# Optimization experiments

Hardware: AMD Instinct MI355X
Metric: run time of the kernel (lower is better)

Reference implementation:

```python
import jax, jax.numpy as jnp
import numpy as np

EMBED_DIM = 1024
NUM_HEADS = 16
HEAD_DIM = EMBED_DIM // NUM_HEADS


def setup_inputs() -> dict:
    key = jax.random.key(0)
    ks = jax.random.split(key, 9)
    B, T, C = 4, 2048, EMBED_DIM
    s = 1.0 / np.sqrt(C)
    return {
        "x": jax.random.normal(ks[0], (B, T, C), jnp.float32),
        "Wq": jax.random.normal(ks[1], (C, C), jnp.float32) * s,
        "bq": jnp.zeros((C,), jnp.float32),
        "Wk": jax.random.normal(ks[2], (C, C), jnp.float32) * s,
        "bk": jnp.zeros((C,), jnp.float32),
        "Wv": jax.random.normal(ks[3], (C, C), jnp.float32) * s,
        "bv": jnp.zeros((C,), jnp.float32),
        "Wo": jax.random.normal(ks[4], (C, C), jnp.float32) * s,
        "bo": jnp.zeros((C,), jnp.float32),
    }


def reference(x, Wq, bq, Wk, bk, Wv, bv, Wo, bo):
    B, T, C = x.shape
    H, D = NUM_HEADS, HEAD_DIM
    # projections (torch Linear: y = x @ W.T + b; here weights stored as [in, out])
    q = (x @ Wq + bq).reshape(B, T, H, D).transpose(0, 2, 1, 3)  # [B,H,T,D]
    k = (x @ Wk + bk).reshape(B, T, H, D).transpose(0, 2, 1, 3)
    v = (x @ Wv + bv).reshape(B, T, H, D).transpose(0, 2, 1, 3)
    scores = jnp.einsum("bhqd,bhkd->bhqk", q, k) / jnp.sqrt(jnp.float32(D))
    causal = jnp.tril(jnp.ones((T, T), bool))
    scores = jnp.where(causal, scores, -jnp.inf)
    attn = jax.nn.softmax(scores, axis=-1)
    out = jnp.einsum("bhqk,bhkd->bhqd", attn, v)  # [B,H,T,D]
    out = out.transpose(0, 2, 1, 3).reshape(B, T, C)
    return out @ Wo + bo
```

## Files before the change

kernel.cpp:

```cpp
#include <hip/hip_runtime.h>
#include <hip/hip_bf16.h>
#include <math.h>

typedef __hip_bfloat16 bf16_t;
typedef __attribute__((ext_vector_type(8))) short short8;
typedef __attribute__((ext_vector_type(4))) float floatx4;

#define T_SEQ 2048
#define NB    4
#define NH    16
#define HD    64
#define C_DIM 1024
#define M_ROWS (NB * T_SEQ)

#define Q_SCALE 0.18033688011f

__device__ __forceinline__ void load_lds16(const bf16_t* g, bf16_t* l) {
    __builtin_amdgcn_global_load_lds(
        (const __attribute__((address_space(1))) void*)g,
        (__attribute__((address_space(3))) void*)l,
        16, 0, 0);
}

__device__ __forceinline__ floatx4 mfma16(short8 a, short8 b, floatx4 c) {
    return __builtin_amdgcn_mfma_f32_16x16x32_bf16(a, b, c, 0, 0, 0);
}

__global__ void convert_x_kernel(const float* __restrict__ x, bf16_t* __restrict__ xb) {
    int i = blockIdx.x * 256 + threadIdx.x;
    float4 v = reinterpret_cast<const float4*>(x)[i];
    union { bf16_t h[4]; short4 s4; } u;
    u.h[0] = __float2bfloat16(v.x);
    u.h[1] = __float2bfloat16(v.y);
    u.h[2] = __float2bfloat16(v.z);
    u.h[3] = __float2bfloat16(v.w);
    reinterpret_cast<short4*>(xb)[i] = u.s4;
}

__global__ void transpose_cvt_kernel(const float* __restrict__ W0, const float* __restrict__ W1,
                                     const float* __restrict__ W2, const float* __restrict__ W3,
                                     bf16_t* __restrict__ O0, bf16_t* __restrict__ O1,
                                     bf16_t* __restrict__ O2, bf16_t* __restrict__ O3) {
    const float* W = (blockIdx.z == 0) ? W0 : (blockIdx.z == 1) ? W1 : (blockIdx.z == 2) ? W2 : W3;
    bf16_t*      O = (blockIdx.z == 0) ? O0 : (blockIdx.z == 1) ? O1 : (blockIdx.z == 2) ? O2 : O3;
    __shared__ float tile[32][33];
    int bx = blockIdx.x * 32, by = blockIdx.y * 32;
    int tx = threadIdx.x, ty = threadIdx.y;
#pragma unroll
    for (int j = 0; j < 32; j += 8)
        tile[ty + j][tx] = W[(size_t)(by + ty + j) * C_DIM + bx + tx];
    __syncthreads();
#pragma unroll
    for (int j = 0; j < 32; j += 8)
        O[(size_t)(bx + ty + j) * C_DIM + by + tx] = __float2bfloat16(tile[tx][ty + j]);
}

__device__ __forceinline__ void gemm_mainloop(const bf16_t* __restrict__ Ablk,
                                              const bf16_t* __restrict__ Bblk,
                                              bf16_t* As, bf16_t* Bs,
                                              floatx4 acc[4][4], int wave, int lane) {
    int lr = lane & 15, lq = lane >> 4;
    int wr = (wave >> 1) * 64, wc = (wave & 1) * 64;
    for (int kt = 0; kt < C_DIM; kt += 64) {
#pragma unroll
        for (int j = 0; j < 4; ++j) {
            int chunk = j * 256 + wave * 64 + lane;
            int r = chunk >> 3, ps = chunk & 7;
            int c = ((ps ^ (r & 7)) * 8);
            load_lds16(Ablk + (size_t)r * C_DIM + kt + c, As + chunk * 8);
            load_lds16(Bblk + (size_t)r * C_DIM + kt + c, Bs + chunk * 8);
        }
        __syncthreads();
#pragma unroll
        for (int kk = 0; kk < 2; ++kk) {
            short8 af[4], bfr[4];
            int psw = ((kk * 4 + lq) ^ (lr & 7)) * 8;
#pragma unroll
            for (int m = 0; m < 4; ++m)
                af[m] = *reinterpret_cast<const short8*>(As + (wr + m * 16 + lr) * 64 + psw);
#pragma unroll
            for (int n = 0; n < 4; ++n)
                bfr[n] = *reinterpret_cast<const short8*>(Bs + (wc + n * 16 + lr) * 64 + psw);
#pragma unroll
            for (int m = 0; m < 4; ++m)
#pragma unroll
                for (int n = 0; n < 4; ++n)
                    acc[m][n] = mfma16(af[m], bfr[n], acc[m][n]);
        }
        __syncthreads();
    }
}

__global__ __launch_bounds__(256, 3) void gemm_qkv_kernel(
    const bf16_t* __restrict__ xb,
    const bf16_t* __restrict__ WqT, const bf16_t* __restrict__ WkT, const bf16_t* __restrict__ WvT,
    const float* __restrict__ bq, const float* __restrict__ bk, const float* __restrict__ bv,
    bf16_t* __restrict__ Q, bf16_t* __restrict__ K, bf16_t* __restrict__ Vt) {
    __shared__ bf16_t As[128 * 64];
    __shared__ bf16_t Bs[128 * 64];
    int tid = threadIdx.x, wave = tid >> 6, lane = tid & 63;

    int f    = (int)blockIdx.x + ((int)blockIdx.y << 3) + ((int)blockIdx.z << 9);
    int xcd  = f & 7;
    int s    = f >> 3;
    int rloc = s & 7;
    int t2   = s >> 3;
    int colp = t2 & 7;
    int wsel = t2 >> 3;
    int row0 = (xcd * 8 + rloc) * 128;
    int col0 = colp * 128;

    const bf16_t* Wt  = (wsel == 0) ? WqT : (wsel == 1) ? WkT : WvT;
    const float* bias = (wsel == 0) ? bq : (wsel == 1) ? bk : bv;

    floatx4 acc[4][4] = {};
    gemm_mainloop(xb + (size_t)row0 * C_DIM, Wt + (size_t)col0 * C_DIM, As, Bs, acc, wave, lane);

    int lr = lane & 15, lq = lane >> 4;
    int wr = (wave >> 1) * 64, wc = (wave & 1) * 64;

    if (wsel == 2) {
#pragma unroll
        for (int nt = 0; nt < 4; ++nt) {
            int col = col0 + wc + nt * 16 + lr;
            float bvv = bias[col];
            int h = col >> 6, d = col & 63;
#pragma unroll
            for (int m = 0; m < 4; ++m) {
                int rowg0 = row0 + wr + m * 16 + lq * 4;
                int b = rowg0 >> 11, t0 = rowg0 & (T_SEQ - 1);
                union { bf16_t h4[4]; short4 s4; } u;
#pragma unroll
                for (int r = 0; r < 4; ++r)
                    u.h4[r] = __float2bfloat16(acc[m][nt][r] + bvv);
                *reinterpret_cast<short4*>(
                    &Vt[((size_t)((b * NH + h) * HD + d)) * T_SEQ + t0]) = u.s4;
            }
        }
    } else {
        float scale = (wsel == 0) ? Q_SCALE : 1.0f;
        bf16_t* outp = (wsel == 0) ? Q : K;
#pragma unroll
        for (int nt = 0; nt < 4; ++nt) {
            int col = col0 + wc + nt * 16 + lr;
            float bvv = bias[col];
            int h = col >> 6, d = col & 63;
#pragma unroll
            for (int m = 0; m < 4; ++m) {
#pragma unroll
                for (int r = 0; r < 4; ++r) {
                    int rowg = row0 + wr + m * 16 + lq * 4 + r;
                    int b = rowg >> 11, t = rowg & (T_SEQ - 1);
                    float val = (acc[m][nt][r] + bvv) * scale;
                    outp[((size_t)((b * NH + h) * T_SEQ + t)) * HD + d] =
                        __float2bfloat16(val);
                }
            }
        }
    }
}

__global__ __launch_bounds__(512, 4) void attn_kernel(
    const bf16_t* __restrict__ Q, const bf16_t* __restrict__ K,
    const bf16_t* __restrict__ Vt, bf16_t* __restrict__ ctx) {
    __shared__ __align__(16) bf16_t Ks[2][64 * 64];
    __shared__ __align__(16) bf16_t Vs[2][64 * 64];
    __shared__ __align__(16) unsigned short Ps[128 * 64];
    int tid = threadIdx.x, w = tid >> 6, lane = tid & 63;
    int lr = lane & 15, lq = lane >> 4;
    int xcd = (int)blockIdx.x;
    int y   = (int)blockIdx.y;
    int bh  = xcd * 8 + (y & 7);
    int qp  = y >> 3;
    int b = bh >> 4, h = bh & 15;

    const bf16_t* Kbase = K  + (size_t)bh * T_SEQ * HD;
    const bf16_t* Vbase = Vt + (size_t)bh * HD * T_SEQ;

#pragma unroll 1
    for (int pass = 0; pass < 2; ++pass) {
        int qt = pass ? qp : (15 - qp);
        int q0 = qt * 128;
        int ktiles = 2 * qt + 2;
        const bf16_t* Qbase = Q + ((size_t)bh * T_SEQ + q0) * HD;

        {
            int ch = tid;
            int r = ch >> 3, ps = ch & 7;
            int c = ((ps ^ (r & 7)) * 8);
            load_lds16(Kbase + (size_t)r * HD + c, Ks[0] + ch * 8);
            load_lds16(Vbase + (size_t)r * T_SEQ + c, Vs[0] + ch * 8);
        }

        short8 qf[2];
#pragma unroll
        for (int kk = 0; kk < 2; ++kk)
            qf[kk] = *reinterpret_cast<const short8*>(
                Qbase + (size_t)(w * 16 + lr) * HD + kk * 32 + lq * 8);

        floatx4 o[4] = {};
        float lpart[4] = {};
        int buf = 0;

        for (int it = 0; it < ktiles; ++it) {
            int kt0 = it * 64;
            __syncthreads();

            if (it + 1 < ktiles) {
                int nk0 = kt0 + 64;
                int ch = tid;
                int r = ch >> 3, ps = ch & 7;
                int c = ((ps ^ (r & 7)) * 8);
                load_lds16(Kbase + (size_t)(nk0 + r) * HD + c, Ks[buf ^ 1] + ch * 8);
                load_lds16(Vbase + (size_t)r * T_SEQ + nk0 + c, Vs[buf ^ 1] + ch * 8);
            }

            const bf16_t* Kc = Ks[buf];
            const bf16_t* Vc = Vs[buf];

            floatx4 s[4] = {};
            short8 kf[4][2];
#pragma unroll
            for (int kk = 0; kk < 2; ++kk) {
                int psw = ((kk * 4 + lq) ^ (lr & 7)) * 8;
#pragma unroll
                for (int n = 0; n < 4; ++n)
                    kf[n][kk] = *reinterpret_cast<const short8*>(Kc + (n * 16 + lr) * 64 + psw);
            }
#pragma unroll
            for (int kk = 0; kk < 2; ++kk)
#pragma unroll
                for (int n = 0; n < 4; ++n)
                    s[n] = mfma16(qf[kk], kf[n][kk], s[n]);

            if (it >= ktiles - 2) {
#pragma unroll
                for (int r = 0; r < 4; ++r) {
                    int rowg = q0 + w * 16 + lq * 4 + r;
#pragma unroll
                    for (int n = 0; n < 4; ++n) {
                        int colg = kt0 + n * 16 + lr;
                        if (colg > rowg) s[n][r] = -1e30f;
                    }
                }
            }

#pragma unroll
            for (int n = 0; n < 4; ++n)
#pragma unroll
                for (int r = 0; r < 4; ++r)
                    s[n][r] = __builtin_amdgcn_exp2f(s[n][r]);
#pragma unroll
            for (int r = 0; r < 4; ++r)
                lpart[r] += (s[0][r] + s[1][r]) + (s[2][r] + s[3][r]);

#pragma unroll
            for (int n = 0; n < 4; ++n)
#pragma unroll
                for (int r = 0; r < 4; ++r) {
                    int prow = w * 16 + lq * 4 + r;
                    int piece = n * 2 + (lr >> 3);
                    union { float f; unsigned u; } cv; cv.f = s[n][r];
                    Ps[prow * 64 + ((piece ^ (prow & 7)) * 8) + (lr & 7)] =
                        (unsigned short)(cv.u >> 16);
                }

            short8 pf[2], vf[4][2];
#pragma unroll
            for (int kk = 0; kk < 2; ++kk) {
                int prow = w * 16 + lr;
                pf[kk] = *reinterpret_cast<const short8*>(
                    Ps + prow * 64 + (((kk * 4 + lq) ^ (lr & 7)) * 8));
            }
#pragma unroll
            for (int kk = 0; kk < 2; ++kk) {
                int psw = ((kk * 4 + lq) ^ (lr & 7)) * 8;
#pragma unroll
                for (int dt = 0; dt < 4; ++dt)
                    vf[dt][kk] = *reinterpret_cast<const short8*>(Vc + (dt * 16 + lr) * 64 + psw);
            }
#pragma unroll
            for (int kk = 0; kk < 2; ++kk)
#pragma unroll
                for (int dt = 0; dt < 4; ++dt)
                    o[dt] = mfma16(pf[kk], vf[dt][kk], o[dt]);

            buf ^= 1;
        }

#pragma unroll
        for (int r = 0; r < 4; ++r) {
            float l = lpart[r];
            l += __shfl_xor(l, 1);
            l += __shfl_xor(l, 2);
            l += __shfl_xor(l, 4);
            l += __shfl_xor(l, 8);
            float inv = 1.0f / l;
            int t = q0 + w * 16 + lq * 4 + r;
#pragma unroll
            for (int dt = 0; dt < 4; ++dt) {
                int d = dt * 16 + lr;
                ctx[((size_t)(b * T_SEQ + t)) * C_DIM + h * HD + d] =
                    __float2bfloat16(o[dt][r] * inv);
            }
        }
    }
}

__global__ __launch_bounds__(256, 3) void gemm_out_kernel(
    const bf16_t* __restrict__ Actx, const bf16_t* __restrict__ WoT,
    const float* __restrict__ bo, float* __restrict__ out) {
    __shared__ bf16_t As[128 * 64];
    __shared__ bf16_t Bs[128 * 64];
    int tid = threadIdx.x, wave = tid >> 6, lane = tid & 63;

    int f    = (int)blockIdx.x + ((int)blockIdx.y << 3);
    int xcd  = f & 7;
    int s    = f >> 3;
    int rloc = s & 7;
    int colp = s >> 3;
    int row0 = (xcd * 8 + rloc) * 128;
    int col0 = colp * 128;

    floatx4 acc[4][4] = {};
    gemm_mainloop(Actx + (size_t)row0 * C_DIM, WoT + (size_t)col0 * C_DIM, As, Bs, acc, wave, lane);
    int lr = lane & 15, lq = lane >> 4;
    int wr = (wave >> 1) * 64, wc = (wave & 1) * 64;
#pragma unroll
    for (int nt = 0; nt < 4; ++nt) {
        int col = col0 + wc + nt * 16 + lr;
        float bvv = bo[col];
#pragma unroll
        for (int m = 0; m < 4; ++m)
#pragma unroll
            for (int r = 0; r < 4; ++r) {
                int rowg = row0 + wr + m * 16 + lq * 4 + r;
                out[(size_t)rowg * C_DIM + col] = acc[m][nt][r] + bvv;
            }
    }
}

extern "C" void kernel_launch(void* const* d_in, const int* in_sizes, int n_in,
                              void* d_out, int out_size, void* d_ws, size_t ws_size,
                              hipStream_t stream) {
    const float* x  = (const float*)d_in[0];
    const float* Wq = (const float*)d_in[1];
    const float* bq = (const float*)d_in[2];
    const float* Wk = (const float*)d_in[3];
    const float* bk = (const float*)d_in[4];
    const float* Wv = (const float*)d_in[5];
    const float* bv = (const float*)d_in[6];
    const float* Wo = (const float*)d_in[7];
    const float* bo = (const float*)d_in[8];
    float* out = (float*)d_out;

    char* ws = (char*)d_ws;
    bf16_t* xb  = (bf16_t*)ws; ws += (size_t)M_ROWS * C_DIM * 2;
    bf16_t* WqT = (bf16_t*)ws; ws += (size_t)C_DIM * C_DIM * 2;
    bf16_t* WkT = (bf16_t*)ws; ws += (size_t)C_DIM * C_DIM * 2;
    bf16_t* WvT = (bf16_t*)ws; ws += (size_t)C_DIM * C_DIM * 2;
    bf16_t* WoT = (bf16_t*)ws; ws += (size_t)C_DIM * C_DIM * 2;
    bf16_t* Qb  = (bf16_t*)ws; ws += (size_t)M_ROWS * C_DIM * 2;
    bf16_t* Kb  = (bf16_t*)ws; ws += (size_t)M_ROWS * C_DIM * 2;
    bf16_t* Vtb = (bf16_t*)ws; ws += (size_t)M_ROWS * C_DIM * 2;
    bf16_t* ctx = (bf16_t*)ws; ws += (size_t)M_ROWS * C_DIM * 2;

    convert_x_kernel<<<(M_ROWS * C_DIM / 4) / 256, 256, 0, stream>>>(x, xb);
    transpose_cvt_kernel<<<dim3(32, 32, 4), dim3(32, 8), 0, stream>>>(
        Wq, Wk, Wv, Wo, WqT, WkT, WvT, WoT);
    gemm_qkv_kernel<<<dim3(8, 64, 3), 256, 0, stream>>>(
        xb, WqT, WkT, WvT, bq, bk, bv, Qb, Kb, Vtb);
    attn_kernel<<<dim3(8, 64), 512, 0, stream>>>(Qb, Kb, Vtb, ctx);
    gemm_out_kernel<<<dim3(8, 64), 256, 0, stream>>>(ctx, WoT, bo, out);
}
```

Baseline: 248.8 us.

## Halve attention block to 4 waves, each computing two 16-row query groups

```diff
diff --git a/kernel.cpp b/kernel.cpp
--- a/kernel.cpp
+++ b/kernel.cpp
@@ -160,7 +160,7 @@
     }
 }
 
-__global__ __launch_bounds__(512, 4) void attn_kernel(
+__global__ __launch_bounds__(256, 2) void attn_kernel(
     const bf16_t* __restrict__ Q, const bf16_t* __restrict__ K,
     const bf16_t* __restrict__ Vt, bf16_t* __restrict__ ctx) {
     __shared__ __align__(16) bf16_t Ks[2][64 * 64];
@@ -184,22 +184,25 @@
         int ktiles = 2 * qt + 2;
         const bf16_t* Qbase = Q + ((size_t)bh * T_SEQ + q0) * HD;
 
-        {
-            int ch = tid;
+#pragma unroll
+        for (int cc = 0; cc < 2; ++cc) {
+            int ch = tid + cc * 256;
             int r = ch >> 3, ps = ch & 7;
             int c = ((ps ^ (r & 7)) * 8);
             load_lds16(Kbase + (size_t)r * HD + c, Ks[0] + ch * 8);
             load_lds16(Vbase + (size_t)r * T_SEQ + c, Vs[0] + ch * 8);
         }
 
-        short8 qf[2];
-#pragma unroll
-        for (int kk = 0; kk < 2; ++kk)
-            qf[kk] = *reinterpret_cast<const short8*>(
-                Qbase + (size_t)(w * 16 + lr) * HD + kk * 32 + lq * 8);
-
-        floatx4 o[4] = {};
-        float lpart[4] = {};
+        short8 qf[2][2];
+#pragma unroll
+        for (int g = 0; g < 2; ++g)
+#pragma unroll
+            for (int kk = 0; kk < 2; ++kk)
+                qf[g][kk] = *reinterpret_cast<const short8*>(
+                    Qbase + (size_t)(w * 32 + g * 16 + lr) * HD + kk * 32 + lq * 8);
+
+        floatx4 o[2][4] = {};
+        float lpart[2][4] = {};
         int buf = 0;
 
         for (int it = 0; it < ktiles; ++it) {
@@ -208,17 +211,20 @@
 
             if (it + 1 < ktiles) {
                 int nk0 = kt0 + 64;
-                int ch = tid;
-                int r = ch >> 3, ps = ch & 7;
-                int c = ((ps ^ (r & 7)) * 8);
-                load_lds16(Kbase + (size_t)(nk0 + r) * HD + c, Ks[buf ^ 1] + ch * 8);
-                load_lds16(Vbase + (size_t)r * T_SEQ + nk0 + c, Vs[buf ^ 1] + ch * 8);
+#pragma unroll
+                for (int cc = 0; cc < 2; ++cc) {
+                    int ch = tid + cc * 256;
+                    int r = ch >> 3, ps = ch & 7;
+                    int c = ((ps ^ (r & 7)) * 8);
+                    load_lds16(Kbase + (size_t)(nk0 + r) * HD + c, Ks[buf ^ 1] + ch * 8);
+                    load_lds16(Vbase + (size_t)r * T_SEQ + nk0 + c, Vs[buf ^ 1] + ch * 8);
+                }
             }
 
             const bf16_t* Kc = Ks[buf];
             const bf16_t* Vc = Vs[buf];
 
-            floatx4 s[4] = {};
+            floatx4 s[2][4] = {};
             short8 kf[4][2];
 #pragma unroll
             for (int kk = 0; kk < 2; ++kk) {
@@ -228,50 +234,61 @@
                     kf[n][kk] = *reinterpret_cast<const short8*>(Kc + (n * 16 + lr) * 64 + psw);
             }
 #pragma unroll
-            for (int kk = 0; kk < 2; ++kk)
+            for (int g = 0; g < 2; ++g)
+#pragma unroll
+                for (int kk = 0; kk < 2; ++kk)
+#pragma unroll
+                    for (int n = 0; n < 4; ++n)
+                        s[g][n] = mfma16(qf[g][kk], kf[n][kk], s[g][n]);
+
+            if (it >= ktiles - 2) {
+#pragma unroll
+                for (int g = 0; g < 2; ++g)
+#pragma unroll
+                    for (int r = 0; r < 4; ++r) {
+                        int rowg = q0 + w * 32 + g * 16 + lq * 4 + r;
+#pragma unroll
+                        for (int n = 0; n < 4; ++n) {
+                            int colg = kt0 + n * 16 + lr;
+                            if (colg > rowg) s[g][n][r] = -1e30f;
+                        }
+                    }
+            }
+
+#pragma unroll
+            for (int g = 0; g < 2; ++g) {
 #pragma unroll
                 for (int n = 0; n < 4; ++n)
-                    s[n] = mfma16(qf[kk], kf[n][kk], s[n]);
-
-            if (it >= ktiles - 2) {
-#pragma unroll
-                for (int r = 0; r < 4; ++r) {
-                    int rowg = q0 + w * 16 + lq * 4 + r;
-#pragma unroll
-                    for (int n = 0; n < 4; ++n) {
-                        int colg = kt0 + n * 16 + lr;
-                        if (colg > rowg) s[n][r] = -1e30f;
+#pragma unroll
+                    for (int r = 0; r < 4; ++r)
+                        s[g][n][r] = __builtin_amdgcn_exp2f(s[g][n][r]);
+#pragma unroll
+                for (int r = 0; r < 4; ++r)
+                    lpart[g][r] += (s[g][0][r] + s[g][1][r]) + (s[g][2][r] + s[g][3][r]);
+            }
+
+#pragma unroll
+            for (int g = 0; g < 2; ++g)
+#pragma unroll
+                for (int n = 0; n < 4; ++n)
+#pragma unroll
+                    for (int r = 0; r < 4; ++r) {
+                        int prow = w * 32 + g * 16 + lq * 4 + r;
+                        int piece = n * 2 + (lr >> 3);
+                        union { float f; unsigned u; } cv; cv.f = s[g][n][r];
+                        Ps[prow * 64 + ((piece ^ (prow & 7)) * 8) + (lr & 7)] =
+                            (unsigned short)(cv.u >> 16);
                     }
+
+            short8 pf[2][2], vf[4][2];
+#pragma unroll
+            for (int g = 0; g < 2; ++g)
+#pragma unroll
+                for (int kk = 0; kk < 2; ++kk) {
+                    int prow = w * 32 + g * 16 + lr;
+                    pf[g][kk] = *reinterpret_cast<const short8*>(
+                        Ps + prow * 64 + (((kk * 4 + lq) ^ (lr & 7)) * 8));
                 }
-            }
-
-#pragma unroll
-            for (int n = 0; n < 4; ++n)
-#pragma unroll
-                for (int r = 0; r < 4; ++r)
-                    s[n][r] = __builtin_amdgcn_exp2f(s[n][r]);
-#pragma unroll
-            for (int r = 0; r < 4; ++r)
-                lpart[r] += (s[0][r] + s[1][r]) + (s[2][r] + s[3][r]);
-
-#pragma unroll
-            for (int n = 0; n < 4; ++n)
-#pragma unroll
-                for (int r = 0; r < 4; ++r) {
-                    int prow = w * 16 + lq * 4 + r;
-                    int piece = n * 2 + (lr >> 3);
-                    union { float f; unsigned u; } cv; cv.f = s[n][r];
-                    Ps[prow * 64 + ((piece ^ (prow & 7)) * 8) + (lr & 7)] =
-                        (unsigned short)(cv.u >> 16);
-                }
-
-            short8 pf[2], vf[4][2];
-#pragma unroll
-            for (int kk = 0; kk < 2; ++kk) {
-                int prow = w * 16 + lr;
-                pf[kk] = *reinterpret_cast<const short8*>(
-                    Ps + prow * 64 + (((kk * 4 + lq) ^ (lr & 7)) * 8));
-            }
 #pragma unroll
             for (int kk = 0; kk < 2; ++kk) {
                 int psw = ((kk * 4 + lq) ^ (lr & 7)) * 8;
@@ -280,30 +297,34 @@
                     vf[dt][kk] = *reinterpret_cast<const short8*>(Vc + (dt * 16 + lr) * 64 + psw);
             }
 #pragma unroll
-            for (int kk = 0; kk < 2; ++kk)
-#pragma unroll
-                for (int dt = 0; dt < 4; ++dt)
-                    o[dt] = mfma16(pf[kk], vf[dt][kk], o[dt]);
+            for (int g = 0; g < 2; ++g)
+#pragma unroll
+                for (int kk = 0; kk < 2; ++kk)
+#pragma unroll
+                    for (int dt = 0; dt < 4; ++dt)
+                        o[g][dt] = mfma16(pf[g][kk], vf[dt][kk], o[g][dt]);
 
             buf ^= 1;
         }
 
 #pragma unroll
-        for (int r = 0; r < 4; ++r) {
-            float l = lpart[r];
-            l += __shfl_xor(l, 1);
-            l += __shfl_xor(l, 2);
-            l += __shfl_xor(l, 4);
-            l += __shfl_xor(l, 8);
-            float inv = 1.0f / l;
-            int t = q0 + w * 16 + lq * 4 + r;
-#pragma unroll
-            for (int dt = 0; dt < 4; ++dt) {
-                int d = dt * 16 + lr;
-                ctx[((size_t)(b * T_SEQ + t)) * C_DIM + h * HD + d] =
-                    __float2bfloat16(o[dt][r] * inv);
-            }
-        }
+        for (int g = 0; g < 2; ++g)
+#pragma unroll
+            for (int r = 0; r < 4; ++r) {
+                float l = lpart[g][r];
+                l += __shfl_xor(l, 1);
+                l += __shfl_xor(l, 2);
+                l += __shfl_xor(l, 4);
+                l += __shfl_xor(l, 8);
+                float inv = 1.0f / l;
+                int t = q0 + w * 32 + g * 16 + lq * 4 + r;
+#pragma unroll
+                for (int dt = 0; dt < 4; ++dt) {
+                    int d = dt * 16 + lr;
+                    ctx[((size_t)(b * T_SEQ + t)) * C_DIM + h * HD + d] =
+                        __float2bfloat16(o[g][dt][r] * inv);
+                }
+            }
     }
 }
 
@@ -370,6 +391,6 @@
         Wq, Wk, Wv, Wo, WqT, WkT, WvT, WoT);
     gemm_qkv_kernel<<<dim3(8, 64, 3), 256, 0, stream>>>(
         xb, WqT, WkT, WvT, bq, bk, bv, Qb, Kb, Vtb);
-    attn_kernel<<<dim3(8, 64), 512, 0, stream>>>(Qb, Kb, Vtb, ctx);
+    attn_kernel<<<dim3(8, 64), 256, 0, stream>>>(Qb, Kb, Vtb, ctx);
     gemm_out_kernel<<<dim3(8, 64), 256, 0, stream>>>(ctx, WoT, bo, out);
 }
```

After: 237.0 us. 1.05x faster.
